# Kernel optimization log

Hardware: AMD Instinct MI355X
Metric: run time of the kernel (lower is better)

## Reference

```python
import jax, jax.numpy as jnp
import numpy as np

UNITS = 256
IN_DIM = 128
BATCH = 128
SEQ = 1024


def setup_inputs() -> dict:
    key = jax.random.key(0)
    k1, k2, k3 = jax.random.split(key, 3)
    x = jax.random.normal(k1, (BATCH, SEQ, IN_DIM), jnp.float32)
    # glorot-ish scale for stability
    input_weight = jax.random.normal(k2, (IN_DIM, 7 * UNITS), jnp.float32) * 0.05
    hidden_weight = jax.random.normal(k3, (UNITS, 3 * UNITS), jnp.float32) * 0.05
    bias = jnp.zeros((3 * UNITS,), jnp.float32)
    # constant = [eye(in_dim); zeros] of shape (units, in_dim), non-trainable
    constant = jnp.concatenate(
        [jnp.eye(IN_DIM, dtype=jnp.float32),
         jnp.zeros((UNITS - IN_DIM, IN_DIM), jnp.float32)], axis=0)
    return {"x": x, "input_weight": input_weight, "hidden_weight": hidden_weight,
            "bias": bias, "constant": constant}


def reference(x, input_weight, hidden_weight, bias, constant):
    u = hidden_weight.shape[0]
    Wxr, Wxu, Wxh, dWxr, dWxu, ddWxr, ddWxu = (
        [input_weight[:, i * u:(i + 1) * u] for i in range(7)])
    Whr, Whu, Whh = [hidden_weight[:, i * u:(i + 1) * u] for i in range(3)]
    br, bu, bh = bias[:u], bias[u:2 * u], bias[2 * u:]

    B = x.shape[0]
    h0 = jnp.zeros((B, u), x.dtype)
    s0 = jnp.zeros((B, u), x.dtype)

    def step(carry, x_t):
        h, s1, s2 = carry
        # recover padded previous inputs: (b,units) @ (units,in) -> (b,in)
        x_tm1 = s1 @ constant
        x_tm2 = s2 @ constant
        d_x = x_t - x_tm1                       # 1st-order finite diff
        dd_x = x_t - 2.0 * x_tm1 + x_tm2        # 2nd-order finite diff
        r = jax.nn.sigmoid(x_t @ Wxr + d_x @ dWxr + dd_x @ ddWxr + h @ Whr + br)
        ug = jax.nn.sigmoid(x_t @ Wxu + d_x @ dWxu + dd_x @ ddWxu + h @ Whu + bu)
        cand = jnp.tanh(x_t @ Wxh + (r * h) @ Whh + bh)
        h_new = ug * h + (1.0 - ug) * cand
        new_s1 = x_t @ constant.T               # pad x_t to units dims
        new_s2 = x_tm1 @ constant.T             # pad x_tm1 to units dims
        return (h_new, new_s1, new_s2), h_new

    xs = jnp.swapaxes(x, 0, 1)                  # (T, B, in_dim)
    _, hs = jax.lax.scan(step, (h0, s0, s0), xs)
    return jnp.swapaxes(hs, 0, 1)               # (B, T, units)
```

## Files before the change

kernel.cpp:

```cpp
#include <hip/hip_runtime.h>

#define SEQL 1024
#define BATCHN 128
#define UNITS 256
#define INDIM 128
#define G3 768

typedef __attribute__((ext_vector_type(8))) short short8;
typedef __attribute__((ext_vector_type(4))) short short4v;
typedef __attribute__((ext_vector_type(4))) float floatx4;

#define NL2E  -1.4426950408889634f
#define PL2E2  2.8853900817779268f

#define HSTRIDE 272

__device__ __forceinline__ short f2bf(float f) {
  unsigned u = __float_as_uint(f);
  u += 0x7fff + ((u >> 16) & 1);
  return (short)(u >> 16);
}
__device__ __forceinline__ float bf2f(unsigned short s) {
  return __uint_as_float(((unsigned)s) << 16);
}
__device__ __forceinline__ float fexp2(float x) {
#if __has_builtin(__builtin_amdgcn_exp2f)
  return __builtin_amdgcn_exp2f(x);
#else
  return __expf(0.6931471805599453f * x);
#endif
}
__device__ __forceinline__ float frcp(float x) {
#if __has_builtin(__builtin_amdgcn_rcpf)
  return __builtin_amdgcn_rcpf(x);
#else
  return 1.f / x;
#endif
}

#define LDS_BARRIER() do {                                   \
    asm volatile("s_waitcnt lgkmcnt(0)" ::: "memory");       \
    __builtin_amdgcn_s_barrier();                            \
    asm volatile("" ::: "memory");                           \
  } while (0)

__device__ __forceinline__ void acq_spin(const int* p) {
  while (__hip_atomic_load(p, __ATOMIC_ACQUIRE, __HIP_MEMORY_SCOPE_AGENT) == 0)
    __builtin_amdgcn_s_sleep(8);
}

__global__ void prep_kernel(const float* __restrict__ iw,
                            const float* __restrict__ hw,
                            short* __restrict__ WcB, short* __restrict__ WhB,
                            int* __restrict__ flags) {
  int idx = blockIdx.x * 256 + threadIdx.x;
  const int WCN = 384 * G3;
  if (idx < WCN) {
    int k = idx / G3, n = idx % G3;
    int i = k & 127, blkk = k >> 7;
    int gsel = n >> 8, c = n & 255;
    const float* row = iw + (size_t)i * 1792;
    float v;
    if (blkk == 0) {
      v = (gsel == 0) ? row[c] + row[768 + c] + row[1280 + c]
        : (gsel == 1) ? row[256 + c] + row[1024 + c] + row[1536 + c]
                      : row[512 + c];
    } else if (blkk == 1) {
      v = (gsel == 0) ? -(row[768 + c] + 2.f * row[1280 + c])
        : (gsel == 1) ? -(row[1024 + c] + 2.f * row[1536 + c])
                      : 0.f;
    } else {
      v = (gsel == 0) ? row[1280 + c]
        : (gsel == 1) ? row[1536 + c]
                      : 0.f;
    }
    v *= (gsel == 2) ? PL2E2 : NL2E;
    int kk = k >> 5, q = (k >> 3) & 3, j = k & 7;
    WcB[(((n * 12 + kk) * 4 + q) * 8) + j] = f2bf(v);
  } else {
    idx -= WCN;
    if (idx < 256 * G3) {
      int k = idx / G3, n = idx % G3;
      float v = hw[(size_t)k * G3 + n] * ((n >> 8) == 2 ? PL2E2 : NL2E);
      int kk = k >> 5, q = (k >> 3) & 3, j = k & 7;
      WhB[(((n * 8 + kk) * 4 + q) * 8) + j] = f2bf(v);
    } else {
      idx -= 256 * G3;
      if (idx < SEQL * 8) flags[idx] = 0;
    }
  }
}

__global__ __launch_bounds__(512, 2) void fused_kernel(
    const float* __restrict__ x, const short* __restrict__ WcB,
    const float* __restrict__ bias, unsigned* __restrict__ pre2,
    const short* __restrict__ WhB, float* __restrict__ out,
    int* __restrict__ flags) {
  __shared__ __align__(16) short smem[12288];

  if (blockIdx.x >= 32) {
    const int pidx = blockIdx.x - 32;
    const int tpair = pidx >> 3, mt = pidx & 7;
    const int tid = threadIdx.x;
    const int half = tid >> 8, htid = tid & 255;
    const int t = tpair * 2 + half;
    short* xF = smem + half * 6144;

#pragma unroll
    for (int it = 0; it < 6; ++it) {
      int rr = it * 8 + (htid >> 5);
      int dt = rr >> 4, bb = rr & 15;
      int lane32 = htid & 31, c = lane32 * 4;
      floatx4 v = {0.f, 0.f, 0.f, 0.f};
      if (t >= dt)
        v = *(const floatx4*)(x + ((size_t)(mt * 16 + bb) * SEQL + (t - dt)) * INDIM + c);
      int kk = dt * 4 + (c >> 5), qq = (c >> 3) & 3, j0 = c & 7;
      short4v pk;
#pragma unroll
      for (int j = 0; j < 4; ++j) pk[j] = f2bf(v[j]);
      *(short4v*)&xF[((kk * 64 + qq * 16 + bb) * 8) + j0] = pk;
    }
    __syncthreads();

    const int wvp = htid >> 6, lane = htid & 63, ln16 = lane & 15;
    const int qp = lane >> 4;

    short8 aF[12];
#pragma unroll
    for (int kk = 0; kk < 12; ++kk) aF[kk] = *(const short8*)&xF[(kk * 64 + lane) * 8];

    unsigned* slab = pre2 + (size_t)((mt * 4 + qp) * SEQL + t) * 1536;

#pragma unroll
    for (int ig = 0; ig < 3; ++ig) {
      const int ngrp = wvp * 3 + ig;
      const float sc = (ngrp >= 8) ? PL2E2 : NL2E;
      floatx4 acc[4];
#pragma unroll
      for (int nt = 0; nt < 4; ++nt) {
        float bv = bias[ngrp * 64 + nt * 16 + ln16] * sc;
#pragma unroll
        for (int r = 0; r < 4; ++r) acc[nt][r] = bv;
      }
#pragma unroll
      for (int kk = 0; kk < 12; ++kk) {
#pragma unroll
        for (int nt = 0; nt < 4; ++nt) {
          int n = ngrp * 64 + nt * 16 + ln16;
          short8 w = *(const short8*)(WcB + (((size_t)(n * 12 + kk) * 4 + qp) * 8));
          acc[nt] = __builtin_amdgcn_mfma_f32_16x16x32_bf16(aF[kk], w, acc[nt], 0, 0, 0);
        }
      }
      const int g = ngrp >> 2;
#pragma unroll
      for (int p = 0; p < 2; ++p) {
        int wvc = (ngrp & 3) * 2 + p;
#pragma unroll
        for (int r = 0; r < 4; ++r) {
          unsigned lo = (unsigned)(unsigned short)f2bf(acc[2 * p][r]);
          unsigned hi = (unsigned)(unsigned short)f2bf(acc[2 * p + 1][r]);
          slab[g * 512 + wvc * 64 + r * 16 + ln16] = lo | (hi << 16);
        }
      }
    }

    __syncthreads();
    if (tid == 0) {
      __threadfence();
      __hip_atomic_store(&flags[(2 * tpair) * 8 + mt], 1,
                         __ATOMIC_RELEASE, __HIP_MEMORY_SCOPE_AGENT);
      __hip_atomic_store(&flags[(2 * tpair + 1) * 8 + mt], 1,
                         __ATOMIC_RELEASE, __HIP_MEMORY_SCOPE_AGENT);
    }
    return;
  }

  __builtin_amdgcn_s_setprio(2);

  short* hFc = smem;
  short* rFc = smem + 4 * HSTRIDE;

  const int tid = threadIdx.x;
  const int wv = tid >> 6, lane = tid & 63, ln16 = lane & 15, q = lane >> 4;
  const int row4 = lane & 3;
  const int wg = blockIdx.x;
  const int mtg = wg >> 2;

  short8 wR[2][8], wU[2][8], wH[2][8];
#pragma unroll
  for (int nt = 0; nt < 2; ++nt) {
    int nr = wv * 32 + nt * 16 + ln16;
#pragma unroll
    for (int kk = 0; kk < 8; ++kk) {
      wR[nt][kk] = *(const short8*)(WhB + (((size_t)(nr * 8 + kk) * 4 + q) * 8));
      wU[nt][kk] = *(const short8*)(WhB + (((size_t)((256 + nr) * 8 + kk) * 4 + q) * 8));
      wH[nt][kk] = *(const short8*)(WhB + (((size_t)((512 + nr) * 8 + kk) * 4 + q) * 8));
    }
  }
  for (int i = tid; i < 4 * HSTRIDE; i += 512) { hFc[i] = 0; rFc[i] = 0; }

  const floatx4 z4 = {0.f, 0.f, 0.f, 0.f};
  float hq[2] = {0.f, 0.f};

  const unsigned* slab0 = pre2 + (size_t)wg * SEQL * 1536;

  acq_spin(&flags[0 * 8 + mtg]);
  unsigned cur0 = slab0[0 * 512 + tid];
  unsigned cur1 = slab0[1 * 512 + tid];
  unsigned cur2 = slab0[2 * 512 + tid];
  int fcur = __hip_atomic_load(&flags[1 * 8 + mtg],
                               __ATOMIC_RELAXED, __HIP_MEMORY_SCOPE_AGENT);

  float* outBase = out + ((size_t)(wg * 4 + q) * SEQL) * UNITS + wv * 32 + ln16;
  const int aoff = row4 * HSTRIDE + q * 8;
  const int woff = q * HSTRIDE + wv * 32 + ln16;

  __syncthreads();

  for (int t = 0; t < SEQL; ++t) {
    int fnxt = 1;
    if (t + 2 < SEQL)
      fnxt = __hip_atomic_load(&flags[(t + 2) * 8 + mtg],
                               __ATOMIC_RELAXED, __HIP_MEMORY_SCOPE_AGENT);
    if (t + 1 < SEQL && fcur == 0) acq_spin(&flags[(t + 1) * 8 + mtg]);
    asm volatile("" ::: "memory");

    const unsigned* nslab = slab0 + (size_t)(t < SEQL - 1 ? t + 1 : t) * 1536;
    unsigned nxt0 = nslab[0 * 512 + tid];
    unsigned nxt1 = nslab[1 * 512 + tid];
    unsigned nxt2 = nslab[2 * 512 + tid];

    floatx4 accR[2], accU[2];
    {
      const short8 a0 = *(const short8*)&hFc[aoff];
      accR[0] = __builtin_amdgcn_mfma_f32_16x16x32_bf16(a0, wR[0][0], z4, 0, 0, 0);
      accR[1] = __builtin_amdgcn_mfma_f32_16x16x32_bf16(a0, wR[1][0], z4, 0, 0, 0);
      accU[0] = __builtin_amdgcn_mfma_f32_16x16x32_bf16(a0, wU[0][0], z4, 0, 0, 0);
      accU[1] = __builtin_amdgcn_mfma_f32_16x16x32_bf16(a0, wU[1][0], z4, 0, 0, 0);
    }
#pragma unroll
    for (int kk = 1; kk < 8; ++kk) {
      const short8 a = *(const short8*)&hFc[aoff + kk * 32];
      accR[0] = __builtin_amdgcn_mfma_f32_16x16x32_bf16(a, wR[0][kk], accR[0], 0, 0, 0);
      accR[1] = __builtin_amdgcn_mfma_f32_16x16x32_bf16(a, wR[1][kk], accR[1], 0, 0, 0);
      accU[0] = __builtin_amdgcn_mfma_f32_16x16x32_bf16(a, wU[0][kk], accU[0], 0, 0, 0);
      accU[1] = __builtin_amdgcn_mfma_f32_16x16x32_bf16(a, wU[1][kk], accU[1], 0, 0, 0);
    }
    float uq[2];
#pragma unroll
    for (int nt = 0; nt < 2; ++nt) {
      float vR = (q == 0) ? accR[nt][0] : (q == 1) ? accR[nt][1]
               : (q == 2) ? accR[nt][2] : accR[nt][3];
      float vU = (q == 0) ? accU[nt][0] : (q == 1) ? accU[nt][1]
               : (q == 2) ? accU[nt][2] : accU[nt][3];
      float pR = bf2f((unsigned short)(nt ? (cur0 >> 16) : (cur0 & 0xffff)));
      float pU = bf2f((unsigned short)(nt ? (cur1 >> 16) : (cur1 & 0xffff)));
      float rg = frcp(1.f + fexp2(vR + pR));
      uq[nt]   = frcp(1.f + fexp2(vU + pU));
      rFc[woff + nt * 16] = f2bf(rg * hq[nt]);
    }
    LDS_BARRIER();

    floatx4 accH[2];
    {
      const short8 a0 = *(const short8*)&rFc[aoff];
      accH[0] = __builtin_amdgcn_mfma_f32_16x16x32_bf16(a0, wH[0][0], z4, 0, 0, 0);
      accH[1] = __builtin_amdgcn_mfma_f32_16x16x32_bf16(a0, wH[1][0], z4, 0, 0, 0);
    }
#pragma unroll
    for (int kk = 1; kk < 8; ++kk) {
      const short8 a = *(const short8*)&rFc[aoff + kk * 32];
      accH[0] = __builtin_amdgcn_mfma_f32_16x16x32_bf16(a, wH[0][kk], accH[0], 0, 0, 0);
      accH[1] = __builtin_amdgcn_mfma_f32_16x16x32_bf16(a, wH[1][kk], accH[1], 0, 0, 0);
    }
#pragma unroll
    for (int nt = 0; nt < 2; ++nt) {
      float vH = (q == 0) ? accH[nt][0] : (q == 1) ? accH[nt][1]
               : (q == 2) ? accH[nt][2] : accH[nt][3];
      float pH = bf2f((unsigned short)(nt ? (cur2 >> 16) : (cur2 & 0xffff)));
      float cand = 1.f - 2.f * frcp(1.f + fexp2(vH + pH));
      float hnew = uq[nt] * (hq[nt] - cand) + cand;
      hq[nt] = hnew;
      hFc[woff + nt * 16] = f2bf(hnew);
      outBase[(size_t)t * UNITS + nt * 16] = hnew;
    }
    cur0 = nxt0; cur1 = nxt1; cur2 = nxt2; fcur = fnxt;
    LDS_BARRIER();
  }
}

extern "C" void kernel_launch(void* const* d_in, const int* in_sizes, int n_in,
                              void* d_out, int out_size, void* d_ws, size_t ws_size,
                              hipStream_t stream) {
  const float* x    = (const float*)d_in[0];
  const float* iw   = (const float*)d_in[1];
  const float* hw   = (const float*)d_in[2];
  const float* bias = (const float*)d_in[3];
  float* out = (float*)d_out;

  unsigned* pre2 = (unsigned*)d_ws;
  const size_t preDwords = (size_t)32 * SEQL * 1536;
  short* WcB = (short*)(pre2 + preDwords);
  short* WhB = WcB + (size_t)384 * G3;
  int* flags = (int*)(WhB + (size_t)256 * G3);

  prep_kernel<<<1952, 256, 0, stream>>>(iw, hw, WcB, WhB, flags);
  fused_kernel<<<32 + 4096, 512, 0, stream>>>(x, WcB, bias, pre2, WhB, out, flags);
}
```

Measured before the change: 1.573 ms.

## Steer producer blocks off recurrent-block CUs using a dynamic work queue

```diff
diff --git a/kernel.cpp b/kernel.cpp
--- a/kernel.cpp
+++ b/kernel.cpp
@@ -14,6 +14,14 @@
 #define PL2E2  2.8853900817779268f
 
 #define HSTRIDE 272
+
+#define C_HEAD 0
+#define C_TAIL 1
+#define C_RDY  3
+#define C_KEY  4
+#define C_PROG 36
+#define TAIL_CAP 48
+#define PARK_MARGIN 128
 
 __device__ __forceinline__ short f2bf(float f) {
   unsigned u = __float_as_uint(f);
@@ -47,6 +55,14 @@
 __device__ __forceinline__ void acq_spin(const int* p) {
   while (__hip_atomic_load(p, __ATOMIC_ACQUIRE, __HIP_MEMORY_SCOPE_AGENT) == 0)
     __builtin_amdgcn_s_sleep(8);
+}
+
+__device__ __forceinline__ unsigned cu_key() {
+  unsigned hwid, xcc;
+  asm volatile("s_getreg_b32 %0, hwreg(4)\n\t"
+               "s_getreg_b32 %1, hwreg(20)"
+               : "=s"(hwid), "=s"(xcc));
+  return ((xcc & 0xffu) << 16) | (hwid & 0xff00u);
 }
 
 __global__ void prep_kernel(const float* __restrict__ iw,
@@ -86,7 +102,7 @@
       WhB[(((n * 8 + kk) * 4 + q) * 8) + j] = f2bf(v);
     } else {
       idx -= 256 * G3;
-      if (idx < SEQL * 8) flags[idx] = 0;
+      if (idx < SEQL * 8 + 128) flags[idx] = 0;
     }
   }
 }
@@ -97,11 +113,60 @@
     const short* __restrict__ WhB, float* __restrict__ out,
     int* __restrict__ flags) {
   __shared__ __align__(16) short smem[12288];
+  __shared__ int bctl[2];
+  int* ctl = flags + SEQL * 8;
 
   if (blockIdx.x >= 32) {
-    const int pidx = blockIdx.x - 32;
-    const int tpair = pidx >> 3, mt = pidx & 7;
     const int tid = threadIdx.x;
+    if (tid == 0) {
+      for (int it = 0; it < 2000; ++it) {
+        if (__hip_atomic_load(&ctl[C_RDY], __ATOMIC_ACQUIRE,
+                              __HIP_MEMORY_SCOPE_AGENT) >= 32) break;
+        __builtin_amdgcn_s_sleep(2);
+      }
+      unsigned k = cu_key();
+      int polite = 0;
+      for (int i = 0; i < 32; ++i)
+        if ((unsigned)__hip_atomic_load(&ctl[C_KEY + i], __ATOMIC_RELAXED,
+                                        __HIP_MEMORY_SCOPE_AGENT) == k)
+          polite = 1;
+      int item;
+      if (polite) {
+        int n = __hip_atomic_fetch_add(&ctl[C_TAIL], 1, __ATOMIC_RELAXED,
+                                       __HIP_MEMORY_SCOPE_AGENT);
+        if (n < TAIL_CAP) {
+          item = 4095 - n;
+        } else {
+          polite = 0;
+          item = __hip_atomic_fetch_add(&ctl[C_HEAD], 1, __ATOMIC_RELAXED,
+                                        __HIP_MEMORY_SCOPE_AGENT);
+        }
+      } else {
+        item = __hip_atomic_fetch_add(&ctl[C_HEAD], 1, __ATOMIC_RELAXED,
+                                      __HIP_MEMORY_SCOPE_AGENT);
+      }
+      bctl[0] = item; bctl[1] = polite;
+    }
+    __syncthreads();
+    const int item = bctl[0];
+    const int tpair = item >> 3, mt = item & 7;
+
+    if (bctl[1]) {
+      if (tid == 0) {
+        const int thr = 2 * tpair - PARK_MARGIN;
+        for (int it = 0; it < (1 << 20); ++it) {
+          int m0 = __hip_atomic_load(&ctl[C_PROG + mt * 4 + 0], __ATOMIC_RELAXED, __HIP_MEMORY_SCOPE_AGENT);
+          int m1 = __hip_atomic_load(&ctl[C_PROG + mt * 4 + 1], __ATOMIC_RELAXED, __HIP_MEMORY_SCOPE_AGENT);
+          int m2 = __hip_atomic_load(&ctl[C_PROG + mt * 4 + 2], __ATOMIC_RELAXED, __HIP_MEMORY_SCOPE_AGENT);
+          int m3 = __hip_atomic_load(&ctl[C_PROG + mt * 4 + 3], __ATOMIC_RELAXED, __HIP_MEMORY_SCOPE_AGENT);
+          int m = min(min(m0, m1), min(m2, m3));
+          if (m >= thr) break;
+          __builtin_amdgcn_s_sleep(8);
+        }
+      }
+      __syncthreads();
+    }
+
     const int half = tid >> 8, htid = tid & 255;
     const int t = tpair * 2 + half;
     short* xF = smem + half * 6144;
@@ -175,15 +240,24 @@
     return;
   }
 
+  const int tid = threadIdx.x;
+  const int wg = blockIdx.x;
+
+  if (tid == 0) {
+    unsigned k = cu_key();
+    __hip_atomic_store(&ctl[C_KEY + wg], (int)k, __ATOMIC_RELAXED,
+                       __HIP_MEMORY_SCOPE_AGENT);
+    __hip_atomic_fetch_add(&ctl[C_RDY], 1, __ATOMIC_RELEASE,
+                           __HIP_MEMORY_SCOPE_AGENT);
+  }
+
   __builtin_amdgcn_s_setprio(2);
 
   short* hFc = smem;
   short* rFc = smem + 4 * HSTRIDE;
 
-  const int tid = threadIdx.x;
   const int wv = tid >> 6, lane = tid & 63, ln16 = lane & 15, q = lane >> 4;
   const int row4 = lane & 3;
-  const int wg = blockIdx.x;
   const int mtg = wg >> 2;
 
   short8 wR[2][8], wU[2][8], wH[2][8];
@@ -218,6 +292,9 @@
   __syncthreads();
 
   for (int t = 0; t < SEQL; ++t) {
+    if (tid == 0)
+      __hip_atomic_store(&ctl[C_PROG + wg], t, __ATOMIC_RELAXED,
+                         __HIP_MEMORY_SCOPE_AGENT);
     int fnxt = 1;
     if (t + 2 < SEQL)
       fnxt = __hip_atomic_load(&flags[(t + 2) * 8 + mtg],
@@ -304,6 +381,6 @@
   short* WhB = WcB + (size_t)384 * G3;
   int* flags = (int*)(WhB + (size_t)256 * G3);
 
-  prep_kernel<<<1952, 256, 0, stream>>>(iw, hw, WcB, WhB, flags);
+  prep_kernel<<<1953, 256, 0, stream>>>(iw, hw, WcB, WhB, flags);
   fused_kernel<<<32 + 4096, 512, 0, stream>>>(x, WcB, bias, pre2, WhB, out, flags);
 }
```

New measurement: 1.627 ms. 3.4% more time.
